# Performance work log

Measured on AMD Instinct MI355X. Metric: run time of the kernel, lower is better.

Reference implementation:

```python
import jax, jax.numpy as jnp
import numpy as np

N_CLASSES = 16384
M = 2
D = 128


def setup_inputs() -> dict:
    key = jax.random.key(0)
    k1, k2 = jax.random.split(key)
    x = jax.random.normal(k1, (N_CLASSES * M, D), dtype=jnp.float32)
    anchor_idx = jax.random.randint(k2, (N_CLASSES,), 0, M, dtype=jnp.int64 if jax.config.jax_enable_x64 else jnp.int32).astype(jnp.int32)
    pos_idx = (1 - anchor_idx).astype(jnp.int32)  # randperm(2) -> positive is the other sample
    return {"x": x, "anchor_idx": anchor_idx, "pos_idx": pos_idx}


def reference(x, anchor_idx, pos_idx):
    # x: [N*M, D]; anchor_idx/pos_idx: [N] in [0, M)
    N = anchor_idx.shape[0]
    Dx = x.shape[1]
    xr = x.reshape(N, M, Dx)
    anchors = jnp.take_along_axis(xr, anchor_idx[:, None, None], axis=1)[:, 0, :]    # [N, D]
    positives = jnp.take_along_axis(xr, pos_idx[:, None, None], axis=1)[:, 0, :]     # [N, D]
    negs = xr[:, 1, :]                                                               # [N, D] (sample 1 of every class)
    # score[i, j] = a_i . (neg_j - pos_i) = a_i . neg_j - a_i . pos_i
    S = anchors @ negs.T                                                             # [N, N]
    ap = jnp.sum(anchors * positives, axis=1)                                        # [N]
    logits = S - ap[:, None]
    mask = ~jnp.eye(N, dtype=bool)                                                   # exclude j == i (own class)
    sums = jnp.sum(jnp.where(mask, jnp.exp(logits), jnp.float32(0.0)), axis=1)       # [N]
    return jnp.sum(jnp.log1p(sums))
```

## Files before the change

### kernel.cpp

```cpp
#include <hip/hip_runtime.h>
#include <hip/hip_bf16.h>
#include <math.h>

#define N_CLS 16384
#define DDIM  128
#define CSHIFT 50.0f
#define LOG2E 1.4426950408889634f
#define NEGC2 (-72.13475204444817f)

#if __has_builtin(__builtin_amdgcn_exp2f)
#define EXP2(x) __builtin_amdgcn_exp2f(x)
#else
#define EXP2(x) exp2f(x)
#endif

typedef __attribute__((ext_vector_type(8))) short short8;
typedef __attribute__((ext_vector_type(4))) float f32x4;

__device__ __forceinline__ unsigned short f2bf(float f) {
    __hip_bfloat16 h = __float2bfloat16(f);
    return *(unsigned short*)&h;
}

__global__ __launch_bounds__(256)
void prep_kernel(const float* __restrict__ x,
                 const int* __restrict__ aidx,
                 float* __restrict__ ap,
                 unsigned short* __restrict__ Afrag,
                 unsigned short* __restrict__ Bfrag,
                 float* __restrict__ out) {
    const int t = threadIdx.x;
    const int l = t & 31;
    const int i = blockIdx.x * 8 + (t >> 5);
    const float4 xa = *(const float4*)(x + (2L * i) * DDIM + l * 4);
    const float4 xb = *(const float4*)(x + (2L * i + 1) * DDIM + l * 4);
    const float4 av = (aidx[i] == 0) ? xa : xb;

    const int kc = l >> 3, q = (l >> 1) & 3, j0 = (l & 1) * 4;
    const long base = ((long)((i >> 4) * 4 + kc)) * 512 + (q * 16 + (i & 15)) * 8 + j0;

    ushort4 a4;
    a4.x = f2bf(av.x * LOG2E); a4.y = f2bf(av.y * LOG2E);
    a4.z = f2bf(av.z * LOG2E); a4.w = f2bf(av.w * LOG2E);
    *(ushort4*)(Afrag + base) = a4;

    ushort4 b4;
    b4.x = f2bf(xb.x); b4.y = f2bf(xb.y); b4.z = f2bf(xb.z); b4.w = f2bf(xb.w);
    *(ushort4*)(Bfrag + base) = b4;

    float d = xa.x * xb.x + xa.y * xb.y + xa.z * xb.z + xa.w * xb.w;
    d += __shfl_xor(d, 1, 64);
    d += __shfl_xor(d, 2, 64);
    d += __shfl_xor(d, 4, 64);
    d += __shfl_xor(d, 8, 64);
    d += __shfl_xor(d, 16, 64);
    if (l == 0) ap[i] = d;
    if (blockIdx.x == 0 && t == 0) out[0] = 0.0f;
}

__global__ __launch_bounds__(256, 2)
void fused_kernel(const unsigned short* __restrict__ Afrag,
                  const unsigned short* __restrict__ Bfrag,
                  float* __restrict__ partial) {
    const int tid = threadIdx.x;
    const int lane = tid & 63;
    const int w = tid >> 6;
    const int quad = lane >> 4;
    const int l15 = lane & 15;
    const int oct = blockIdx.x & 7;
    const int rt = blockIdx.x >> 3;
    const int wm2 = w >> 1;
    const int wh = w & 1;

    short8 af[4][4];
    {
        const unsigned short* abase =
            Afrag + ((long)(rt * 8 + wm2 * 4) * 4) * 512 + lane * 8;
        #pragma unroll
        for (int mt = 0; mt < 4; ++mt)
            #pragma unroll
            for (int kc = 0; kc < 4; ++kc)
                af[mt][kc] = *(const short8*)(abase + (mt * 4 + kc) * 512);
    }

    const unsigned short* bbase =
        Bfrag + ((long)(oct * 128 + wh * 4) * 4) * 512 + lane * 8;

    float rs[4][4] = {};
    short8 bA[4], bB[4];
    #pragma unroll
    for (int nt = 0; nt < 4; ++nt)
        bA[nt] = *(const short8*)(bbase + nt * 4 * 512);

    for (int it = 0; it < 16; ++it) {
        const long itoff = (long)it * 16384;
        const long nxoff = (it < 15) ? itoff + 16384 : itoff;

        f32x4 acc[4][4];
        #pragma unroll
        for (int mt = 0; mt < 4; ++mt)
            #pragma unroll
            for (int nt = 0; nt < 4; ++nt)
                acc[mt][nt] = (f32x4){NEGC2, NEGC2, NEGC2, NEGC2};

        #pragma unroll
        for (int nt = 0; nt < 4; ++nt)
            bB[nt] = *(const short8*)(bbase + itoff + (nt * 4 + 1) * 512);
        #pragma unroll
        for (int mt = 0; mt < 4; ++mt)
            #pragma unroll
            for (int nt = 0; nt < 4; ++nt)
                acc[mt][nt] = __builtin_amdgcn_mfma_f32_16x16x32_bf16(
                    af[mt][0], bA[nt], acc[mt][nt], 0, 0, 0);

        #pragma unroll
        for (int nt = 0; nt < 4; ++nt)
            bA[nt] = *(const short8*)(bbase + itoff + (nt * 4 + 2) * 512);
        #pragma unroll
        for (int mt = 0; mt < 4; ++mt)
            #pragma unroll
            for (int nt = 0; nt < 4; ++nt)
                acc[mt][nt] = __builtin_amdgcn_mfma_f32_16x16x32_bf16(
                    af[mt][1], bB[nt], acc[mt][nt], 0, 0, 0);

        #pragma unroll
        for (int nt = 0; nt < 4; ++nt)
            bB[nt] = *(const short8*)(bbase + itoff + (nt * 4 + 3) * 512);
        #pragma unroll
        for (int mt = 0; mt < 4; ++mt)
            #pragma unroll
            for (int nt = 0; nt < 4; ++nt)
                acc[mt][nt] = __builtin_amdgcn_mfma_f32_16x16x32_bf16(
                    af[mt][2], bA[nt], acc[mt][nt], 0, 0, 0);

        #pragma unroll
        for (int nt = 0; nt < 4; ++nt)
            bA[nt] = *(const short8*)(bbase + nxoff + nt * 4 * 512);
        #pragma unroll
        for (int mt = 0; mt < 4; ++mt)
            #pragma unroll
            for (int nt = 0; nt < 4; ++nt)
                acc[mt][nt] = __builtin_amdgcn_mfma_f32_16x16x32_bf16(
                    af[mt][3], bB[nt], acc[mt][nt], 0, 0, 0);

        const int ct = oct * 16 + it;
        if (ct == rt) {
            #pragma unroll
            for (int mt = 0; mt < 4; ++mt)
                #pragma unroll
                for (int nt = 0; nt < 4; ++nt)
                    #pragma unroll
                    for (int reg = 0; reg < 4; ++reg) {
                        const bool diag = (wm2 == wh) && (mt == nt) &&
                                          (quad * 4 + reg == l15);
                        const float e = EXP2(acc[mt][nt][reg]);
                        rs[mt][reg] += diag ? 0.0f : e;
                    }
        } else {
            #pragma unroll
            for (int mt = 0; mt < 4; ++mt)
                #pragma unroll
                for (int nt = 0; nt < 4; ++nt)
                    #pragma unroll
                    for (int reg = 0; reg < 4; ++reg)
                        rs[mt][reg] += EXP2(acc[mt][nt][reg]);
        }
    }

    const int slot = oct * 2 + wh;
    const int rowBase = rt * 128 + wm2 * 64;
    #pragma unroll
    for (int mt = 0; mt < 4; ++mt)
        #pragma unroll
        for (int reg = 0; reg < 4; ++reg) {
            float v = rs[mt][reg];
            v += __shfl_xor(v, 1, 64);
            v += __shfl_xor(v, 2, 64);
            v += __shfl_xor(v, 4, 64);
            v += __shfl_xor(v, 8, 64);
            if (l15 == 0)
                partial[(long)slot * N_CLS + rowBase + mt * 16 + quad * 4 + reg] = v;
        }
}

__global__ __launch_bounds__(256)
void finalize_kernel(const float* __restrict__ partial,
                     const float* __restrict__ ap,
                     float* __restrict__ out) {
    __shared__ float red[256];
    const int t = threadIdx.x;
    const int row = blockIdx.x * 256 + t;
    float s = 0.0f;
    #pragma unroll
    for (int p = 0; p < 16; ++p) s += partial[(long)p * N_CLS + row];
    const float u = logf(s) + (CSHIFT - ap[row]);
    const float loss = (u > 25.0f) ? u : log1pf(__expf(u));
    red[t] = loss;
    __syncthreads();
    for (int st = 128; st > 0; st >>= 1) {
        if (t < st) red[t] += red[t + st];
        __syncthreads();
    }
    if (t == 0) atomicAdd(out, red[0]);
}

extern "C" void kernel_launch(void* const* d_in, const int* in_sizes, int n_in,
                              void* d_out, int out_size, void* d_ws, size_t ws_size,
                              hipStream_t stream) {
    const float* x    = (const float*)d_in[0];
    const int*   aidx = (const int*)d_in[1];

    char* ws = (char*)d_ws;
    float* ap             = (float*)(ws);
    float* partial        = (float*)(ws + 131072);
    unsigned short* Afrag = (unsigned short*)(ws + 131072 + 1048576);
    unsigned short* Bfrag = (unsigned short*)(ws + 131072 + 1048576 + 4194304);

    prep_kernel<<<N_CLS / 8, 256, 0, stream>>>(x, aidx, ap, Afrag, Bfrag, (float*)d_out);
    fused_kernel<<<1024, 256, 0, stream>>>(Afrag, Bfrag, partial);
    finalize_kernel<<<64, 256, 0, stream>>>(partial, ap, (float*)d_out);
}
```

Baseline: 142.7 us.

## Software-pipeline MFMA over N-subtiles with ping-pong accumulators to overlap exp epilogue

Restructures the inner loop to compute one 16-column subtile at a time across all K chunks, using two ping-pong accumulator sets. The exp2 epilogue of the previous subtile is interleaved with the MFMAs of the next, so transcendental work overlaps matrix work. This also cuts live accumulator registers from 16 to 8 vectors. The diagonal mask is now applied per subtile via a precomputed iteration index. B-fragment loads change order to K-major per subtile, which may alter the memory access pattern.

```diff
diff --git a/kernel.cpp b/kernel.cpp
--- a/kernel.cpp
+++ b/kernel.cpp
@@ -86,86 +86,81 @@
     const unsigned short* bbase =
         Bfrag + ((long)(oct * 128 + wh * 4) * 4) * 512 + lane * 8;
 
+    const f32x4 cinit = (f32x4){NEGC2, NEGC2, NEGC2, NEGC2};
     float rs[4][4] = {};
-    short8 bA[4], bB[4];
+    short8 bP[4], bQ[4];
+    f32x4 accA[4], accB[4];
+
+    const bool canDiag = ((rt >> 4) == oct) && (wm2 == wh);
+    const int itd = canDiag ? (rt & 15) : -1;
+
+    auto mfma4 = [&](f32x4 (&acc)[4], short8 (&b)[4]) {
+        #pragma unroll
+        for (int mt = 0; mt < 4; ++mt)
+            acc[mt] = __builtin_amdgcn_mfma_f32_16x16x32_bf16(
+                af[mt][0], b[0], cinit, 0, 0, 0);
+        #pragma unroll
+        for (int kc = 1; kc < 4; ++kc)
+            #pragma unroll
+            for (int mt = 0; mt < 4; ++mt)
+                acc[mt] = __builtin_amdgcn_mfma_f32_16x16x32_bf16(
+                    af[mt][kc], b[kc], acc[mt], 0, 0, 0);
+    };
+    auto epi = [&](f32x4 (&acc)[4]) {
+        #pragma unroll
+        for (int mt = 0; mt < 4; ++mt)
+            #pragma unroll
+            for (int reg = 0; reg < 4; ++reg)
+                rs[mt][reg] += EXP2(acc[mt][reg]);
+    };
+    auto epiD = [&](f32x4 (&acc)[4], int nt) {
+        #pragma unroll
+        for (int mt = 0; mt < 4; ++mt)
+            #pragma unroll
+            for (int reg = 0; reg < 4; ++reg) {
+                float e = EXP2(acc[mt][reg]);
+                if (mt == nt) e = (quad * 4 + reg == l15) ? 0.0f : e;
+                rs[mt][reg] += e;
+            }
+    };
+
     #pragma unroll
-    for (int nt = 0; nt < 4; ++nt)
-        bA[nt] = *(const short8*)(bbase + nt * 4 * 512);
-
+    for (int kc = 0; kc < 4; ++kc)
+        bP[kc] = *(const short8*)(bbase + kc * 512);
+
+    bool dprev = false;
     for (int it = 0; it < 16; ++it) {
-        const long itoff = (long)it * 16384;
-        const long nxoff = (it < 15) ? itoff + 16384 : itoff;
-
-        f32x4 acc[4][4];
-        #pragma unroll
-        for (int mt = 0; mt < 4; ++mt)
-            #pragma unroll
-            for (int nt = 0; nt < 4; ++nt)
-                acc[mt][nt] = (f32x4){NEGC2, NEGC2, NEGC2, NEGC2};
-
-        #pragma unroll
-        for (int nt = 0; nt < 4; ++nt)
-            bB[nt] = *(const short8*)(bbase + itoff + (nt * 4 + 1) * 512);
-        #pragma unroll
-        for (int mt = 0; mt < 4; ++mt)
-            #pragma unroll
-            for (int nt = 0; nt < 4; ++nt)
-                acc[mt][nt] = __builtin_amdgcn_mfma_f32_16x16x32_bf16(
-                    af[mt][0], bA[nt], acc[mt][nt], 0, 0, 0);
-
-        #pragma unroll
-        for (int nt = 0; nt < 4; ++nt)
-            bA[nt] = *(const short8*)(bbase + itoff + (nt * 4 + 2) * 512);
-        #pragma unroll
-        for (int mt = 0; mt < 4; ++mt)
-            #pragma unroll
-            for (int nt = 0; nt < 4; ++nt)
-                acc[mt][nt] = __builtin_amdgcn_mfma_f32_16x16x32_bf16(
-                    af[mt][1], bB[nt], acc[mt][nt], 0, 0, 0);
-
-        #pragma unroll
-        for (int nt = 0; nt < 4; ++nt)
-            bB[nt] = *(const short8*)(bbase + itoff + (nt * 4 + 3) * 512);
-        #pragma unroll
-        for (int mt = 0; mt < 4; ++mt)
-            #pragma unroll
-            for (int nt = 0; nt < 4; ++nt)
-                acc[mt][nt] = __builtin_amdgcn_mfma_f32_16x16x32_bf16(
-                    af[mt][2], bA[nt], acc[mt][nt], 0, 0, 0);
-
-        #pragma unroll
-        for (int nt = 0; nt < 4; ++nt)
-            bA[nt] = *(const short8*)(bbase + nxoff + nt * 4 * 512);
-        #pragma unroll
-        for (int mt = 0; mt < 4; ++mt)
-            #pragma unroll
-            for (int nt = 0; nt < 4; ++nt)
-                acc[mt][nt] = __builtin_amdgcn_mfma_f32_16x16x32_bf16(
-                    af[mt][3], bB[nt], acc[mt][nt], 0, 0, 0);
-
-        const int ct = oct * 16 + it;
-        if (ct == rt) {
-            #pragma unroll
-            for (int mt = 0; mt < 4; ++mt)
-                #pragma unroll
-                for (int nt = 0; nt < 4; ++nt)
-                    #pragma unroll
-                    for (int reg = 0; reg < 4; ++reg) {
-                        const bool diag = (wm2 == wh) && (mt == nt) &&
-                                          (quad * 4 + reg == l15);
-                        const float e = EXP2(acc[mt][nt][reg]);
-                        rs[mt][reg] += diag ? 0.0f : e;
-                    }
-        } else {
-            #pragma unroll
-            for (int mt = 0; mt < 4; ++mt)
-                #pragma unroll
-                for (int nt = 0; nt < 4; ++nt)
-                    #pragma unroll
-                    for (int reg = 0; reg < 4; ++reg)
-                        rs[mt][reg] += EXP2(acc[mt][nt][reg]);
-        }
+        const unsigned short* p1 = bbase + (long)it * 16384;
+        const bool d = (it == itd);
+
+        #pragma unroll
+        for (int kc = 0; kc < 4; ++kc)
+            bQ[kc] = *(const short8*)(p1 + 2048 + kc * 512);
+        mfma4(accA, bP);
+        if (it > 0) { if (dprev) epiD(accB, 3); else epi(accB); }
+
+        #pragma unroll
+        for (int kc = 0; kc < 4; ++kc)
+            bP[kc] = *(const short8*)(p1 + 4096 + kc * 512);
+        mfma4(accB, bQ);
+        if (d) epiD(accA, 0); else epi(accA);
+
+        #pragma unroll
+        for (int kc = 0; kc < 4; ++kc)
+            bQ[kc] = *(const short8*)(p1 + 6144 + kc * 512);
+        mfma4(accA, bP);
+        if (d) epiD(accB, 1); else epi(accB);
+
+        const unsigned short* p2 = bbase + (long)((it < 15) ? it + 1 : it) * 16384;
+        #pragma unroll
+        for (int kc = 0; kc < 4; ++kc)
+            bP[kc] = *(const short8*)(p2 + kc * 512);
+        mfma4(accB, bQ);
+        if (d) epiD(accA, 2); else epi(accA);
+
+        dprev = d;
     }
+    if (dprev) epiD(accB, 3); else epi(accB);
 
     const int slot = oct * 2 + wh;
     const int rowBase = rt * 128 + wm2 * 64;
```

Result: faster. 139.0 us (-2.6%).
